# Kernel tuning notes

Measured on AMD Instinct MI355X. Metric: run time of the kernel, lower is better.

## Reference

```python
import jax, jax.numpy as jnp
import numpy as np

N_SUBJECTS = 64
N_LABELS = 16
DENS_TEMP = 0.1  # args.ProtoSim_dens_temp


def setup_inputs() -> dict:
    key = jax.random.key(0)
    k1, k2, k3 = jax.random.split(key, 3)
    B, V, D = 16384, 2, 512
    X_data = jax.random.normal(k1, (B, V, D), dtype=jnp.float32)
    subject = jax.random.randint(k2, (B,), 0, N_SUBJECTS)
    labels = jax.random.randint(k3, (B,), 0, N_LABELS)
    return {"X_data": X_data, "subject": subject, "labels": labels}


def reference(X_data, subject, labels):
    B, V, D = X_data.shape  # V == contrast_count == 2 (code doubles subject/labels once)
    K = N_SUBJECTS * N_LABELS
    # torch.cat(torch.unbind(X, dim=1), dim=0) -> [V*B, D]
    cf = jnp.transpose(X_data, (1, 0, 2)).reshape(V * B, D)
    subj2 = jnp.concatenate([subject, subject])
    lab2 = jnp.concatenate([labels, labels])
    # group id: groups enumerated sorted-by-(subject,label), i.e. g = s*C + l
    gid = subj2 * N_LABELS + lab2
    ones = jnp.ones((V * B,), dtype=cf.dtype)
    counts = jax.ops.segment_sum(ones, gid, num_segments=K)  # [K]
    safe_cnt = jnp.maximum(counts, 1.0)
    centroid = jax.ops.segment_sum(cf, gid, num_segments=K) / safe_cnt[:, None]  # [K, D]
    # per-sample euclidean distance to own group centroid (torch.cdist)
    dist = jnp.linalg.norm(cf - centroid[gid], axis=1)  # [V*B]
    # density_g = mean(sqrt(dist)) / log(n_g + 10) for n_g > 1, else dmax; then clip & scale
    mean_sqrt = jax.ops.segment_sum(jnp.sqrt(dist), gid, num_segments=K) / safe_cnt
    density = mean_sqrt / jnp.log(counts + 10.0)
    density = jnp.where(counts > 1, density, 0.0)
    density = jnp.where(counts > 1, density, density.max())
    density = jnp.clip(density, jnp.percentile(density, 10), jnp.percentile(density, 90))
    density = DENS_TEMP * density / density.mean()
    density = jax.lax.stop_gradient(density)  # torch builds it via .tolist()/numpy
    # mask: different subject AND same label vs each group prototype
    g_subj = jnp.arange(K) // N_LABELS
    g_lab = jnp.arange(K) % N_LABELS
    mask = ((subj2[:, None] != g_subj[None, :]) & (lab2[:, None] == g_lab[None, :])).astype(cf.dtype)  # [V*B, K]
    # with N_SUBJECTS > 1 every row has >= 1 positive group -> no rows deleted
    sim = jnp.matmul(cf, centroid.T) / density[None, :]  # [V*B, K]
    sim = sim - jax.lax.stop_gradient(jnp.max(sim, axis=1, keepdims=True))
    positive_sim = sim * mask
    # CrossEntropyLoss(reduction='none') with soft (unnormalized) targets = mask
    logp = jax.nn.log_softmax(positive_sim, axis=1)
    loss_per_row = -(mask * logp).sum(axis=1) / mask.sum(axis=1)
    return loss_per_row.mean()
```

## Files before the change

kernel.cpp:

```cpp
#include <hip/hip_runtime.h>


typedef __bf16 v8bf __attribute__((ext_vector_type(8)));
typedef __bf16 v4bf __attribute__((ext_vector_type(4)));
typedef float  v4f  __attribute__((ext_vector_type(4)));
typedef float  v16f __attribute__((ext_vector_type(16)));
typedef unsigned int u32x4 __attribute__((ext_vector_type(4)));

#define B_ROWS 16384
#define ROWS   32768
#define NGRP   1024
#define DIM    512
#define LOG2E  1.4426950408889634f
#define LN2    0.6931471805599453f

__device__ __forceinline__ float wredSum(float v){
#pragma unroll
  for (int o = 32; o > 0; o >>= 1) v += __shfl_xor(v, o);
  return v;
}
__device__ __forceinline__ float wredMax(float v){
#pragma unroll
  for (int o = 32; o > 0; o >>= 1) v = fmaxf(v, __shfl_xor(v, o));
  return v;
}

__device__ __forceinline__ void gload16(const void* g, void* lds){
  __builtin_amdgcn_global_load_lds(
      (const __attribute__((address_space(1))) void*)g,
      (__attribute__((address_space(3))) void*)lds, 16, 0, 0);
}

__global__ void kA2(const int* __restrict__ subj, const int* __restrict__ lab,
                    int* __restrict__ base_cnt, int* __restrict__ gid_arr){
  int i = blockIdx.x * 256 + threadIdx.x;
  int g = subj[i] * 16 + lab[i];
  gid_arr[i] = g;
  atomicAdd(&base_cnt[g], 1);
}

__global__ void kA3(const int* __restrict__ base_cnt, int* __restrict__ offs,
                    int* __restrict__ fillp){
  __shared__ int sb[NGRP];
  int t = threadIdx.x;
  int c = base_cnt[t];
  sb[t] = c;
  __syncthreads();
  for (int off = 1; off < NGRP; off <<= 1){
    int v = (t >= off) ? sb[t - off] : 0;
    __syncthreads();
    sb[t] += v;
    __syncthreads();
  }
  int ex = sb[t] - c;
  offs[t] = ex;
  fillp[t] = ex;
}

__global__ void kA4(const int* __restrict__ gid_arr, int* __restrict__ fillp,
                    int* __restrict__ row_list){
  int i = blockIdx.x * 256 + threadIdx.x;
  int pos = atomicAdd(&fillp[gid_arr[i]], 1);
  row_list[pos] = i;
}

__global__ void kB(const float* __restrict__ X, const int* __restrict__ base_cnt,
                   const int* __restrict__ offs, const int* __restrict__ row_list,
                   float* __restrict__ cent_f, __bf16* __restrict__ cent_b){
  int g = blockIdx.x, t = threadIdx.x;
  int n = base_cnt[g], off = offs[g];
  float ax = 0.f, ay = 0.f, az = 0.f, aw = 0.f;
  for (int j = 0; j < n; ++j){
    int r = row_list[off + j];
    const float4* p = (const float4*)(X + (size_t)r * 1024);
    float4 a = p[t];
    float4 b = p[t + 128];
    ax += a.x + b.x; ay += a.y + b.y; az += a.z + b.z; aw += a.w + b.w;
  }
  int cnt2 = 2 * n;
  float inv = 1.0f / (float)(cnt2 > 1 ? cnt2 : 1);
  float4 c; c.x = ax * inv; c.y = ay * inv; c.z = az * inv; c.w = aw * inv;
  ((float4*)(cent_f + (size_t)g * DIM))[t] = c;
  v4bf cb; cb[0] = (__bf16)c.x; cb[1] = (__bf16)c.y; cb[2] = (__bf16)c.z; cb[3] = (__bf16)c.w;
  *(v4bf*)(cent_b + (size_t)g * DIM + t * 4) = cb;
}

__global__ void kC(const float* __restrict__ X, const int* __restrict__ subj,
                   const int* __restrict__ lab, const float* __restrict__ cent_f,
                   float* __restrict__ msq, __bf16* __restrict__ cfb){
  int w = threadIdx.x >> 6, lane = threadIdx.x & 63;
  int r = blockIdx.x * 4 + w;
  int i = r & (B_ROWS - 1), v = r >> 14;
  int g = subj[i] * 16 + lab[i];
  const float4* xr = (const float4*)(X + ((size_t)(i * 2 + v)) * DIM);
  const float4* cr = (const float4*)(cent_f + (size_t)g * DIM);
  float4 x0 = xr[lane], x1 = xr[lane + 64];
  float4 c0 = cr[lane], c1 = cr[lane + 64];
  float s = 0.f, d;
  d = x0.x - c0.x; s += d * d;  d = x0.y - c0.y; s += d * d;
  d = x0.z - c0.z; s += d * d;  d = x0.w - c0.w; s += d * d;
  d = x1.x - c1.x; s += d * d;  d = x1.y - c1.y; s += d * d;
  d = x1.z - c1.z; s += d * d;  d = x1.w - c1.w; s += d * d;
  v4bf b0; b0[0]=(__bf16)x0.x; b0[1]=(__bf16)x0.y; b0[2]=(__bf16)x0.z; b0[3]=(__bf16)x0.w;
  v4bf b1; b1[0]=(__bf16)x1.x; b1[1]=(__bf16)x1.y; b1[2]=(__bf16)x1.z; b1[3]=(__bf16)x1.w;
  *(v4bf*)(cfb + (size_t)r * DIM + lane * 4)       = b0;
  *(v4bf*)(cfb + (size_t)r * DIM + 256 + lane * 4) = b1;
  s = wredSum(s);
  if (lane == 0){
    float dist = sqrtf(s);
    atomicAdd(&msq[g], sqrtf(dist));
  }
}

__global__ void kD(const int* __restrict__ base_cnt, const float* __restrict__ msq,
                   float* __restrict__ scale2){
  __shared__ float sd[NGRP];
  __shared__ float ss[NGRP];
  __shared__ float rb[16];
  int t = threadIdx.x;
  int lane = t & 63, wid = t >> 6;
  int cnt2 = 2 * base_cnt[t];
  float safe = (float)(cnt2 > 1 ? cnt2 : 1);
  float v = (msq[t] / safe) / logf((float)cnt2 + 10.0f);
  float d1 = (cnt2 > 1) ? v : 0.0f;
  float wm = wredMax(d1);
  if (lane == 0) rb[wid] = wm;
  __syncthreads();
  float x = (lane < 16) ? rb[lane] : -3.0e38f;
  if (wid == 0){ x = wredMax(x); if (lane == 0) rb[0] = x; }
  __syncthreads();
  float dmax = rb[0];
  float d2 = (cnt2 > 1) ? d1 : dmax;
  sd[t] = d2;
  __syncthreads();
  int rank = 0;
  for (int j = 0; j < NGRP; ++j){
    float dj = sd[j];
    rank += (dj < d2) || (dj == d2 && j < t);
  }
  ss[rank] = d2;
  __syncthreads();
  float p10 = ss[102] + 0.3f * (ss[103] - ss[102]);
  float p90 = ss[920] + 0.7f * (ss[921] - ss[920]);
  float c = fminf(fmaxf(d2, p10), p90);
  __syncthreads();
  float wsm = wredSum(c);
  if (lane == 0) rb[wid] = wsm;
  __syncthreads();
  float y = (lane < 16) ? rb[lane] : 0.0f;
  if (wid == 0){ y = wredSum(y); if (lane == 0) rb[0] = y; }
  __syncthreads();
  float mean = rb[0] * (1.0f / 1024.0f);
  scale2[t] = LOG2E * mean / (0.1f * c);
}

__global__ __launch_bounds__(256, 1)
void kE(const __bf16* __restrict__ cfb, const __bf16* __restrict__ centb,
        const float* __restrict__ scale2, const int* __restrict__ gid_arr,
        float* __restrict__ out){
  __shared__ u32x4 tile[2][2048];
  __shared__ float sscale[NGRP];
  __shared__ float redM[128], redE[128], redS[128];
  int tid = threadIdx.x, lane = tid & 63;
  int w = tid >> 6, rw = w & 1, h = w >> 1;
  int l31 = lane & 31, lhi = lane >> 5;
  int row = blockIdx.x * 64 + rw * 32 + l31;

  ((v4f*)sscale)[tid] = ((const v4f*)scale2)[tid];

  u32x4 breg[32];
  {
    const u32x4* rp = (const u32x4*)cfb + (size_t)row * 64 + lhi;
#pragma unroll
    for (int m = 0; m < 32; ++m) breg[m] = rp[2 * m];
  }
  int g0 = gid_arr[row & (B_ROWS - 1)];
  int rsub = g0 >> 4, rlab = g0 & 15;

  const char* gsrc = (const char*)centb;
  auto stage = [&](int t2, int buf){
    int i2 = t2 >> 3, ks2 = t2 & 7;
#pragma unroll
    for (int it = 0; it < 8; ++it){
      int p = it * 256 + tid;
      int trow = p >> 3, clin = p & 7;
      int c = clin ^ (trow & 7);
      int grow = i2 * 128 + (trow & 127) + ((trow >> 7) << 9);
      const void* src = gsrc + ((size_t)(grow * 64 + ks2 * 8 + c) << 4);
      void* dst = (void*)&tile[buf][it * 256 + (w << 6)];
      gload16(src, dst);
    }
  };

  float M = -3.0e38f, E = 0.f, S = 0.f;
  stage(0, 0);
  __syncthreads();

  for (int i = 0; i < 4; ++i){
    v16f acc[4];
#pragma unroll
    for (int fm = 0; fm < 4; ++fm)
#pragma unroll
      for (int e = 0; e < 16; ++e) acc[fm][e] = 0.f;

    for (int ks = 0; ks < 8; ++ks){
      int t2 = i * 8 + ks;
      int buf = t2 & 1;
      if (t2 < 31) stage(t2 + 1, buf ^ 1);
#pragma unroll
      for (int kk = 0; kk < 4; ++kk){
#pragma unroll
        for (int fm = 0; fm < 4; ++fm){
          int tr = h * 128 + fm * 32 + l31;
          u32x4 af = tile[buf][tr * 8 + ((kk * 2 + lhi) ^ (tr & 7))];
          acc[fm] = __builtin_amdgcn_mfma_f32_32x32x16_bf16(
              __builtin_bit_cast(v8bf, af),
              __builtin_bit_cast(v8bf, breg[ks * 4 + kk]),
              acc[fm], 0, 0, 0);
        }
      }
      __syncthreads();
    }

    float mloc = -3.0e38f;
#pragma unroll
    for (int fm = 0; fm < 4; ++fm){
      int sbase = h * 512 + i * 128 + fm * 32 + lhi * 4;
#pragma unroll
      for (int q = 0; q < 4; ++q){
        v4f sc = *(const v4f*)&sscale[sbase + q * 8];
#pragma unroll
        for (int j = 0; j < 4; ++j)
          mloc = fmaxf(mloc, acc[fm][q * 4 + j] * sc[j]);
      }
    }
    float Mn = fmaxf(M, mloc);
    float eadd = 0.f, sadd = 0.f;
#pragma unroll
    for (int fm = 0; fm < 4; ++fm){
      int sbase = h * 512 + i * 128 + fm * 32 + lhi * 4;
      int gs_base = h * 32 + i * 8 + fm * 2;
#pragma unroll
      for (int q = 0; q < 4; ++q){
        v4f sc = *(const v4f*)&sscale[sbase + q * 8];
        float subne = ((gs_base + (q >> 1)) != rsub) ? 1.0f : 0.0f;
#pragma unroll
        for (int j = 0; j < 4; ++j){
          int glab = j + ((q & 1) << 3) + (lhi << 2);
          float mk = (glab == rlab) ? subne : 0.0f;
          float vv = acc[fm][q * 4 + j] * sc[j];
          eadd += mk * exp2f(vv - Mn);
          sadd += mk * vv;
        }
      }
    }
    E = E * exp2f(M - Mn) + eadd;
    S += sadd;
    M = Mn;
  }

  {
    float mo = __shfl_xor(M, 32), eo = __shfl_xor(E, 32), so = __shfl_xor(S, 32);
    float mn = fmaxf(M, mo);
    E = E * exp2f(M - mn) + eo * exp2f(mo - mn);
    S += so; M = mn;
  }
  if (lhi == 0){
    redM[w * 32 + l31] = M; redE[w * 32 + l31] = E; redS[w * 32 + l31] = S;
  }
  __syncthreads();
  if (tid < 64){
    float m0 = redM[tid], e0 = redE[tid], s0 = redS[tid];
    float m1 = redM[tid + 64], e1 = redE[tid + 64], s1 = redS[tid + 64];
    float mn = fmaxf(m0, m1);
    float Ee = e0 * exp2f(m0 - mn) + e1 * exp2f(m1 - mn);
    float Ss = s0 + s1;
    float loss = logf(961.0f + Ee) + LN2 * mn - LN2 * (Ss * (1.0f / 63.0f));
    float ws = wredSum(loss);
    if (tid == 0) atomicAdd(out, ws * (1.0f / (float)ROWS));
  }
}

extern "C" void kernel_launch(void* const* d_in, const int* in_sizes, int n_in,
                              void* d_out, int out_size, void* d_ws, size_t ws_size,
                              hipStream_t stream){
  const float* X   = (const float*)d_in[0];
  const int* subj  = (const int*)d_in[1];
  const int* lab   = (const int*)d_in[2];
  char* ws = (char*)d_ws;

  int*    base_cnt = (int*)(ws + 0);
  float*  msq      = (float*)(ws + 4096);
  int*    offs     = (int*)(ws + 8192);
  int*    fillp    = (int*)(ws + 12288);
  int*    gid_arr  = (int*)(ws + 16384);
  int*    row_list = (int*)(ws + 81920);
  float*  scale2   = (float*)(ws + 147456);
  float*  cent_f   = (float*)(ws + 151552);
  __bf16* cent_b   = (__bf16*)(ws + 2248704);
  __bf16* cfb      = (__bf16*)(ws + 3297280);

  hipMemsetAsync(ws, 0, 8192, stream);
  hipMemsetAsync(d_out, 0, sizeof(float), stream);

  kA2<<<64, 256, 0, stream>>>(subj, lab, base_cnt, gid_arr);
  kA3<<<1, 1024, 0, stream>>>(base_cnt, offs, fillp);
  kA4<<<64, 256, 0, stream>>>(gid_arr, fillp, row_list);
  kB <<<NGRP, 128, 0, stream>>>(X, base_cnt, offs, row_list, cent_f, cent_b);
  kC <<<8192, 256, 0, stream>>>(X, subj, lab, cent_f, msq, cfb);
  kD <<<1, 1024, 0, stream>>>(base_cnt, msq, scale2);
  kE <<<512, 256, 0, stream>>>(cfb, cent_b, scale2, gid_arr, (float*)d_out);
}
```

Before: 182.7 us.

## Replace syncthreads with vmcnt-gated barriers and select masked logits before exp

Replaces __syncthreads around the double-buffered centroid staging with explicit s_waitcnt vmcnt plus raw s_barrier and sched_barriers. This lets the next tile's global loads stay in flight while the current tile is consumed, and the ks loop is now fully unrolled. The softmax epilogue stores the scaled logits back into the accumulators and picks only the lane-relevant masked entries via selects. That cuts the exp2 calls from 64 to 8 per fragment group. The hand-written waitcnt counts depend on the exact number of loads per stage, so a mismatch could cause a race.

```diff
diff --git a/kernel.cpp b/kernel.cpp
--- a/kernel.cpp
+++ b/kernel.cpp
@@ -176,6 +176,9 @@
   }
   int g0 = gid_arr[row & (B_ROWS - 1)];
   int rsub = g0 >> 4, rlab = g0 & 15;
+  int jm = rlab & 3;
+  bool qm1 = (rlab >> 3) & 1;
+  bool lhi_ok = ((rlab >> 2) & 1) == lhi;
 
   const char* gsrc = (const char*)centb;
   auto stage = [&](int t2, int buf){
@@ -194,7 +197,10 @@
 
   float M = -3.0e38f, E = 0.f, S = 0.f;
   stage(0, 0);
-  __syncthreads();
+  asm volatile("s_waitcnt vmcnt(0) lgkmcnt(0)" ::: "memory");
+  __builtin_amdgcn_sched_barrier(0);
+  __builtin_amdgcn_s_barrier();
+  __builtin_amdgcn_sched_barrier(0);
 
   for (int i = 0; i < 4; ++i){
     v16f acc[4];
@@ -203,10 +209,19 @@
 #pragma unroll
       for (int e = 0; e < 16; ++e) acc[fm][e] = 0.f;
 
+#pragma unroll
     for (int ks = 0; ks < 8; ++ks){
       int t2 = i * 8 + ks;
       int buf = t2 & 1;
-      if (t2 < 31) stage(t2 + 1, buf ^ 1);
+      if (t2 < 31){
+        stage(t2 + 1, buf ^ 1);
+        asm volatile("s_waitcnt vmcnt(8)" ::: "memory");
+      } else {
+        asm volatile("s_waitcnt vmcnt(0)" ::: "memory");
+      }
+      __builtin_amdgcn_sched_barrier(0);
+      __builtin_amdgcn_s_barrier();
+      __builtin_amdgcn_sched_barrier(0);
 #pragma unroll
       for (int kk = 0; kk < 4; ++kk){
 #pragma unroll
@@ -219,7 +234,9 @@
               acc[fm], 0, 0, 0);
         }
       }
-      __syncthreads();
+      __builtin_amdgcn_sched_barrier(0);
+      __builtin_amdgcn_s_barrier();
+      __builtin_amdgcn_sched_barrier(0);
     }
 
     float mloc = -3.0e38f;
@@ -230,29 +247,28 @@
       for (int q = 0; q < 4; ++q){
         v4f sc = *(const v4f*)&sscale[sbase + q * 8];
 #pragma unroll
-        for (int j = 0; j < 4; ++j)
-          mloc = fmaxf(mloc, acc[fm][q * 4 + j] * sc[j]);
+        for (int j = 0; j < 4; ++j){
+          float vv = acc[fm][q * 4 + j] * sc[j];
+          acc[fm][q * 4 + j] = vv;
+          mloc = fmaxf(mloc, vv);
+        }
       }
     }
     float Mn = fmaxf(M, mloc);
     float eadd = 0.f, sadd = 0.f;
 #pragma unroll
     for (int fm = 0; fm < 4; ++fm){
-      int sbase = h * 512 + i * 128 + fm * 32 + lhi * 4;
-      int gs_base = h * 32 + i * 8 + fm * 2;
-#pragma unroll
-      for (int q = 0; q < 4; ++q){
-        v4f sc = *(const v4f*)&sscale[sbase + q * 8];
-        float subne = ((gs_base + (q >> 1)) != rsub) ? 1.0f : 0.0f;
-#pragma unroll
-        for (int j = 0; j < 4; ++j){
-          int glab = j + ((q & 1) << 3) + (lhi << 2);
-          float mk = (glab == rlab) ? subne : 0.0f;
-          float vv = acc[fm][q * 4 + j] * sc[j];
-          eadd += mk * exp2f(vv - Mn);
-          sadd += mk * vv;
-        }
-      }
+      float t0 = (jm == 0) ? acc[fm][0]  : (jm == 1) ? acc[fm][1]  : (jm == 2) ? acc[fm][2]  : acc[fm][3];
+      float t1 = (jm == 0) ? acc[fm][4]  : (jm == 1) ? acc[fm][5]  : (jm == 2) ? acc[fm][6]  : acc[fm][7];
+      float t2s= (jm == 0) ? acc[fm][8]  : (jm == 1) ? acc[fm][9]  : (jm == 2) ? acc[fm][10] : acc[fm][11];
+      float t3 = (jm == 0) ? acc[fm][12] : (jm == 1) ? acc[fm][13] : (jm == 2) ? acc[fm][14] : acc[fm][15];
+      float u0 = qm1 ? t1 : t0;
+      float u1 = qm1 ? t3 : t2s;
+      int gs = h * 32 + i * 8 + fm * 2;
+      float m0 = (lhi_ok && (gs     != rsub)) ? 1.0f : 0.0f;
+      float m1 = (lhi_ok && (gs + 1 != rsub)) ? 1.0f : 0.0f;
+      eadd += m0 * exp2f(u0 - Mn) + m1 * exp2f(u1 - Mn);
+      sadd += m0 * u0 + m1 * u1;
     }
     E = E * exp2f(M - Mn) + eadd;
     S += sadd;
```

New measurement: 173.1 us. 1.06x faster.
